# Performance work log

Measured on AMD Instinct MI355X. Metric: run time of the kernel, lower is better.

The kernel has to match this reference:

```python
import jax, jax.numpy as jnp
import numpy as np

THETA = 10000.0  # RoPE base


def _rope(x):
    # x: [B, T, H] with H even. Matches torch view_as_complex on (..., H//2, 2)
    # pairing of adjacent elements, rotated by m * theta_i.
    B, T, H = x.shape
    inv_freq = 1.0 / (THETA ** (jnp.arange(0, H, 2, dtype=jnp.float32) / H))  # [H/2]
    ang = jnp.arange(T, dtype=jnp.float32)[:, None] * inv_freq[None, :]       # [T, H/2]
    cos, sin = jnp.cos(ang), jnp.sin(ang)
    xr = x.astype(jnp.float32).reshape(B, T, H // 2, 2)
    a, b = xr[..., 0], xr[..., 1]
    out = jnp.stack([a * cos - b * sin, a * sin + b * cos], axis=-1)          # complex mult
    return out.reshape(B, T, H).astype(x.dtype)


def setup_inputs() -> dict:
    key = jax.random.key(0)
    k1, k2, k3, k4 = jax.random.split(key, 4)
    B, T, C, H = 4, 4096, 1024, 64
    return {
        "x": jax.random.normal(k1, (B, T, C), dtype=jnp.float32),
        "wq": jax.random.normal(k2, (C, H), dtype=jnp.float32) * 0.02,
        "wk": jax.random.normal(k3, (C, H), dtype=jnp.float32) * 0.02,
        "wv": jax.random.normal(k4, (C, H), dtype=jnp.float32) * 0.02,
    }


def reference(x, wq, wk, wv):
    # Head.forward, training branch; dropout is identity (eval determinism).
    B, T, C = x.shape
    H = wq.shape[1]
    q = _rope(x @ wq)   # [B, T, H]
    k = _rope(x @ wk)   # [B, T, H]
    v = x @ wv          # [B, T, H]
    wei = jnp.einsum('bqh,bkh->bqk', q, k) * (H ** -0.5)   # [B, T, T]
    causal = jnp.tril(jnp.ones((T, T), dtype=bool))
    wei = jnp.where(causal, wei, -jnp.inf)
    wei = jax.nn.softmax(wei, axis=-1)
    out = jnp.einsum('bqk,bkh->bqh', wei, v)               # [B, T, H]
    return out
```

## Files before the change

kernel.cpp:

```cpp
#include <hip/hip_runtime.h>
#include <hip/hip_bf16.h>
#include <math.h>

#define B_ 4
#define T_ 4096
#define C_ 1024
#define H_ 64
#define ROWS_ (B_*T_)

typedef __attribute__((ext_vector_type(8))) short bf16x8;
typedef __attribute__((ext_vector_type(4))) float f32x4;

__device__ __forceinline__ unsigned short f2bf(float f) {
    union { float f; unsigned u; } x; x.f = f;
    unsigned r = x.u + 0x7fffu + ((x.u >> 16) & 1u);
    return (unsigned short)(r >> 16);
}
__device__ __forceinline__ float bf2f(unsigned short s) {
    union { unsigned u; float f; } x; x.u = ((unsigned)s) << 16;
    return x.f;
}
__device__ __forceinline__ unsigned pk2bf(float a, float b) {
    __hip_bfloat162 h = __float22bfloat162_rn(float2{a, b});
    return *reinterpret_cast<unsigned*>(&h);
}
__device__ __forceinline__ void gld16(const void* g, void* l) {
    __builtin_amdgcn_global_load_lds(
        (const __attribute__((address_space(1))) unsigned*)g,
        (__attribute__((address_space(3))) unsigned*)l, 16, 0, 0);
}

__global__ __launch_bounds__(256) void prep_weights(
    const float* __restrict__ wq, const float* __restrict__ wk,
    const float* __restrict__ wv, unsigned short* __restrict__ wt)
{
    __shared__ float ts[64][68];
    const int m  = blockIdx.x >> 4;
    const int k0 = (blockIdx.x & 15) * 64;
    const float* w = (m == 0) ? wq : (m == 1) ? wk : wv;
    const int tid = threadIdx.x;
    {
        const int r = tid >> 2;
        const int c = (tid & 3) * 16;
        #pragma unroll
        for (int i = 0; i < 4; ++i)
            *reinterpret_cast<float4*>(&ts[r][c + 4*i]) =
                *reinterpret_cast<const float4*>(&w[(size_t)(k0 + r)*H_ + c + 4*i]);
    }
    __syncthreads();
    {
        const int n  = tid >> 2;
        const int kc = (tid & 3) * 16;
        unsigned short outp[16];
        #pragma unroll
        for (int j = 0; j < 16; ++j) outp[j] = f2bf(ts[kc + j][n]);
        unsigned short* dst = &wt[((size_t)m*64 + n)*C_ + k0 + kc];
        *reinterpret_cast<uint4*>(dst)     = *reinterpret_cast<uint4*>(&outp[0]);
        *reinterpret_cast<uint4*>(dst + 8) = *reinterpret_cast<uint4*>(&outp[8]);
    }
}

__global__ __launch_bounds__(256) void rope_table_kernel(float* __restrict__ tab)
{
    const int idx = blockIdx.x*256 + threadIdx.x;
    const int t   = idx >> 5;
    const int hp  = idx & 31;
    const float inv = __builtin_exp2f(-(float)hp * (13.287712379549449f / 32.f));
    float sn, cs;
    sincosf((float)t * inv, &sn, &cs);
    *reinterpret_cast<float2*>(&tab[2*idx]) = float2{cs, sn};
}

__global__ __launch_bounds__(512, 2) void qkv_mfma_kernel(
    const float* __restrict__ x, const unsigned short* __restrict__ wt,
    const float* __restrict__ tab,
    unsigned short* __restrict__ qb, unsigned short* __restrict__ kb,
    unsigned short* __restrict__ vtb)
{
    __shared__ unsigned short SM[32768];

    const int tid  = threadIdx.x;
    const int w    = tid >> 6;
    const int lane = tid & 63;
    const int rt   = w >> 1;
    const int ch   = w & 1;
    const int lr   = lane & 15;
    const int lg   = lane >> 4;
    const int rb   = blockIdx.x * 64;

    const int ar = tid >> 3;
    const int ac = (tid & 7) * 8;

    float4 axr[2];

    auto load_A = [&](int t) {
        const float* p = &x[(size_t)(rb + ar)*C_ + t*64 + ac];
        axr[0] = *reinterpret_cast<const float4*>(p);
        axr[1] = *reinterpret_cast<const float4*>(p + 4);
    };
    auto write_A = [&](int buf) {
        unsigned tmp[4];
        tmp[0] = pk2bf(axr[0].x, axr[0].y);
        tmp[1] = pk2bf(axr[0].z, axr[0].w);
        tmp[2] = pk2bf(axr[1].x, axr[1].y);
        tmp[3] = pk2bf(axr[1].z, axr[1].w);
        const int off = buf*8192 + ar*128 + ((ac*2) ^ ((ar & 7) << 4));
        *reinterpret_cast<uint4*>((char*)SM + off) = *reinterpret_cast<uint4*>(tmp);
    };
    auto stage_W = [&](int t, int buf) {
        #pragma unroll
        for (int s = 0; s < 3; ++s) {
            const int slot = s*512 + tid;
            const int r    = slot >> 3;
            const int c8   = (slot & 7) * 8;
            const int c8s  = c8 ^ ((r & 7) << 3);
            gld16(&wt[(size_t)r*C_ + t*64 + c8s],
                  (char*)SM + 16384 + buf*24576 + slot*16);
        }
    };

    f32x4 acc[6];
    #pragma unroll
    for (int j = 0; j < 6; ++j) acc[j] = f32x4{0.f, 0.f, 0.f, 0.f};

    load_A(0);
    stage_W(0, 0);
    write_A(0);
    load_A(1);

    for (int t = 0; t < 16; ++t) {
        const int cur = t & 1, nxt = cur ^ 1;
        __syncthreads();
        if (t < 15) { stage_W(t + 1, nxt); write_A(nxt); }
        if (t < 14) load_A(t + 2);
        char* Acur = (char*)SM + cur*8192;
        char* Wcur = (char*)SM + 16384 + cur*24576;
        #pragma unroll
        for (int kh = 0; kh < 2; ++kh) {
            const int arow = rt*16 + lr;
            bf16x8 af = *reinterpret_cast<const bf16x8*>(
                Acur + arow*128 + ((kh*64 + lg*16) ^ ((arow & 7) << 4)));
            #pragma unroll
            for (int j = 0; j < 6; ++j) {
                const int n = ch*96 + j*16 + lr;
                bf16x8 bf = *reinterpret_cast<const bf16x8*>(
                    Wcur + n*128 + ((kh*64 + lg*16) ^ ((n & 7) << 4)));
                acc[j] = __builtin_amdgcn_mfma_f32_16x16x32_bf16(af, bf, acc[j], 0, 0, 0);
            }
        }
    }

    __syncthreads();
    const int rl0  = rt*16 + lg*4;
    const int row0 = rb + rl0;
    #pragma unroll
    for (int j = 0; j < 6; ++j) {
        const int c = ch*96 + j*16 + lr;
        const int m = c >> 6;
        const int h = c & 63;
        if (m < 2) {
            const int base_ls = (m == 0) ? 0 : 4096;
            const float qs = (m == 0) ? 0.125f : 1.0f;
            const int hp = h >> 1;
            #pragma unroll
            for (int i = 0; i < 4; ++i) {
                const float v  = acc[j][i];
                const float pr = __shfl_xor(v, 1);
                if (!(h & 1)) {
                    const int tp = (row0 + i) & (T_ - 1);
                    const float2 cssn = *reinterpret_cast<const float2*>(
                        &tab[((size_t)tp*32 + hp)*2]);
                    const float oe = (v*cssn.x - pr*cssn.y) * qs;
                    const float oo = (v*cssn.y + pr*cssn.x) * qs;
                    *reinterpret_cast<unsigned*>(&SM[base_ls + (rl0 + i)*64 + h]) =
                        pk2bf(oe, oo);
                }
            }
        } else {
            unsigned short pk[4];
            #pragma unroll
            for (int i = 0; i < 4; ++i) pk[i] = f2bf(acc[j][i]);
            char* vbase = (char*)SM + 16384 + h*128;
            *reinterpret_cast<uint2*>(vbase + ((rl0*2) ^ ((h & 7) << 3))) =
                *reinterpret_cast<uint2*>(pk);
        }
    }
    __syncthreads();
    {
        const int row = tid >> 3;
        const int h0  = (tid & 7) * 8;
        *reinterpret_cast<uint4*>(&qb[(size_t)(rb + row)*H_ + h0]) =
            *reinterpret_cast<const uint4*>(&SM[row*64 + h0]);
        *reinterpret_cast<uint4*>(&kb[(size_t)(rb + row)*H_ + h0]) =
            *reinterpret_cast<const uint4*>(&SM[4096 + row*64 + h0]);
        const int h  = tid >> 3;
        const int t0 = (tid & 7) * 8;
        char* vbase = (char*)SM + 16384 + h*128;
        uint2 a  = *reinterpret_cast<uint2*>(vbase + (((t0*2)    ) ^ ((h & 7) << 3)));
        uint2 b2 = *reinterpret_cast<uint2*>(vbase + (((t0*2) + 8) ^ ((h & 7) << 3)));
        const int bh  = (rb >> 12)*64 + h;
        const int tp0 = rb & (T_ - 1);
        uint4 o; o.x = a.x; o.y = a.y; o.z = b2.x; o.w = b2.y;
        *reinterpret_cast<uint4*>(&vtb[(size_t)bh*T_ + tp0 + t0]) = o;
    }
}

__global__ __launch_bounds__(256, 4) void attn_chunk_kernel(
    const unsigned short* __restrict__ qb, const unsigned short* __restrict__ kb,
    const unsigned short* __restrict__ vtb,
    unsigned short* __restrict__ partO, float* __restrict__ partML,
    int CH, int per_batch)
{
    __shared__ unsigned short Kls[2][4096];
    __shared__ unsigned short Vls[2][4096];
    __shared__ unsigned short Pls[4][1024];

    const int tid  = threadIdx.x;
    const int w    = tid >> 6;
    const int lane = tid & 63;
    const int lr   = lane & 15;
    const int lg   = lane >> 4;

    const int cid = blockIdx.x;
    const int b   = cid / per_batch;
    int r0 = cid - b*per_batch;
    int g = 0, off = 0;
    while (r0 >= off + CH*(g + 1)) { off += CH*(g + 1); ++g; }
    const int idx = r0 - off;
    const int qt  = g*CH + idx/(g + 1);
    const int c   = idx % (g + 1);

    const int q0  = qt * 64;
    const int kt0 = c * CH;
    const int ns  = min(kt0 + CH, qt + 1) - kt0;
    const size_t rbase = (size_t)b * T_;

    char* Pw = (char*)&Pls[w][0];

    bf16x8 qf[2];
    {
        const unsigned short* qp = qb + (rbase + q0 + w*16 + lr)*H_ + lg*8;
        qf[0] = *reinterpret_cast<const bf16x8*>(qp);
        qf[1] = *reinterpret_cast<const bf16x8*>(qp + 32);
    }

    float mrow = -1e30f, lrow = 0.f;
    f32x4 acc[4];
    #pragma unroll
    for (int hs = 0; hs < 4; ++hs) acc[hs] = f32x4{0.f, 0.f, 0.f, 0.f};

    const int srow = tid >> 3;
    const int scol = (tid & 7) * 8;
    auto stage_dma = [&](int kt, int buf) {
        #pragma unroll
        for (int s = 0; s < 2; ++s) {
            const int r    = s*32 + srow;
            const int c8s  = scol ^ ((r & 7) << 3);
            const int slot = s*256 + tid;
            gld16(&kb[(rbase + (size_t)kt*64 + r)*H_ + c8s],
                  (char*)&Kls[buf][0] + slot*16);
            gld16(&vtb[((size_t)(b*64 + r))*T_ + (size_t)kt*64 + c8s],
                  (char*)&Vls[buf][0] + slot*16);
        }
    };

    stage_dma(kt0, 0);

    for (int s = 0; s < ns; ++s) {
        __syncthreads();
        if (s + 1 < ns) stage_dma(kt0 + s + 1, (s + 1) & 1);
        const int kt = kt0 + s;
        char* Kb = (char*)&Kls[s & 1][0];
        char* Vb = (char*)&Vls[s & 1][0];

        f32x4 st[4];
        __builtin_amdgcn_s_setprio(1);
        #pragma unroll
        for (int ks = 0; ks < 4; ++ks) {
            const int rr2 = ks*16 + lr;
            const int sw  = (rr2 & 7) << 4;
            bf16x8 kf0 = *reinterpret_cast<const bf16x8*>(Kb + rr2*128 + ((lg*16     ) ^ sw));
            bf16x8 kf1 = *reinterpret_cast<const bf16x8*>(Kb + rr2*128 + ((lg*16 + 64) ^ sw));
            f32x4 t = {0.f, 0.f, 0.f, 0.f};
            t = __builtin_amdgcn_mfma_f32_16x16x32_bf16(kf0, qf[0], t, 0, 0, 0);
            t = __builtin_amdgcn_mfma_f32_16x16x32_bf16(kf1, qf[1], t, 0, 0, 0);
            st[ks] = t;
        }
        __builtin_amdgcn_s_setprio(0);

        const int qg = q0 + w*16 + lr;
        float mx = -1e30f;
        if (kt == qt) {
            #pragma unroll
            for (int ks = 0; ks < 4; ++ks)
                #pragma unroll
                for (int i = 0; i < 4; ++i) {
                    const int kg = kt*64 + ks*16 + lg*4 + i;
                    const float v = (kg <= qg) ? st[ks][i] : -1e30f;
                    st[ks][i] = v;
                    mx = fmaxf(mx, v);
                }
        } else {
            #pragma unroll
            for (int ks = 0; ks < 4; ++ks)
                #pragma unroll
                for (int i = 0; i < 4; ++i) mx = fmaxf(mx, st[ks][i]);
        }
        mx = fmaxf(mx, __shfl_xor(mx, 16));
        mx = fmaxf(mx, __shfl_xor(mx, 32));
        const float mn  = fmaxf(mrow, mx);
        const float scl = __expf(mrow - mn);
        float ls = 0.f;
        #pragma unroll
        for (int ks = 0; ks < 4; ++ks)
            #pragma unroll
            for (int i = 0; i < 4; ++i) {
                const float p = __expf(st[ks][i] - mn);
                st[ks][i] = p;
                ls += p;
            }
        ls += __shfl_xor(ls, 16);
        ls += __shfl_xor(ls, 32);
        lrow = lrow*scl + ls;
        mrow = mn;

        const int swp = (lr & 7) << 4;
        #pragma unroll
        for (int ks = 0; ks < 4; ++ks) {
            const unsigned u0 = pk2bf(st[ks][0], st[ks][1]);
            const unsigned u1 = pk2bf(st[ks][2], st[ks][3]);
            *reinterpret_cast<uint2*>(Pw + lr*128 + ((ks*32 + lg*8) ^ swp)) =
                make_uint2(u0, u1);
        }

        float sclr[4];
        #pragma unroll
        for (int i = 0; i < 4; ++i) sclr[i] = __shfl(scl, lg*4 + i);
        #pragma unroll
        for (int hs = 0; hs < 4; ++hs)
            #pragma unroll
            for (int i = 0; i < 4; ++i) acc[hs][i] *= sclr[i];

        bf16x8 pf0 = *reinterpret_cast<const bf16x8*>(Pw + lr*128 + ((lg*16     ) ^ swp));
        bf16x8 pf1 = *reinterpret_cast<const bf16x8*>(Pw + lr*128 + ((lg*16 + 64) ^ swp));
        __builtin_amdgcn_s_setprio(1);
        #pragma unroll
        for (int hs = 0; hs < 4; ++hs) {
            const int rv  = hs*16 + lr;
            const int swv = (rv & 7) << 4;
            bf16x8 vf0 = *reinterpret_cast<const bf16x8*>(Vb + rv*128 + ((lg*16     ) ^ swv));
            bf16x8 vf1 = *reinterpret_cast<const bf16x8*>(Vb + rv*128 + ((lg*16 + 64) ^ swv));
            acc[hs] = __builtin_amdgcn_mfma_f32_16x16x32_bf16(pf0, vf0, acc[hs], 0, 0, 0);
            acc[hs] = __builtin_amdgcn_mfma_f32_16x16x32_bf16(pf1, vf1, acc[hs], 0, 0, 0);
        }
        __builtin_amdgcn_s_setprio(0);
    }

    const int myrow = w*16 + lr;
    if (lg == 0) {
        partML[(size_t)cid*128 + myrow]      = mrow;
        partML[(size_t)cid*128 + 64 + myrow] = lrow;
    }
    __syncthreads();
    unsigned short* Ols = &Kls[0][0];
    #pragma unroll
    for (int hs = 0; hs < 4; ++hs)
        #pragma unroll
        for (int i = 0; i < 4; ++i)
            Ols[(w*16 + lg*4 + i)*64 + hs*16 + lr] = f2bf(acc[hs][i]);
    __syncthreads();
    {
        const int e0 = tid * 16;
        *reinterpret_cast<uint4*>(&partO[(size_t)cid*4096 + e0]) =
            *reinterpret_cast<const uint4*>(&Ols[e0]);
        *reinterpret_cast<uint4*>(&partO[(size_t)cid*4096 + e0 + 8]) =
            *reinterpret_cast<const uint4*>(&Ols[e0 + 8]);
    }
}

__global__ __launch_bounds__(256) void combine_kernel(
    const unsigned short* __restrict__ partO, const float* __restrict__ partML,
    float* __restrict__ out, int CH, int per_batch)
{
    const int bq = blockIdx.x;
    const int b  = bq >> 6;
    const int qt = bq & 63;
    const int g  = qt / CH;
    const int nc = g + 1;
    const int cb = b*per_batch + (CH/2)*g*(g + 1) + (qt - g*CH)*(g + 1);

    const int tid = threadIdx.x;
    const int row = tid >> 2;
    const int h0  = (tid & 3) * 16;

    float mi[8], wi[8];
    float M = -1e30f;
    #pragma unroll
    for (int i = 0; i < 8; ++i) if (i < nc) {
        mi[i] = partML[(size_t)(cb + i)*128 + row];
        M = fmaxf(M, mi[i]);
    }
    float L = 0.f;
    #pragma unroll
    for (int i = 0; i < 8; ++i) if (i < nc) {
        wi[i] = __expf(mi[i] - M);
        L += partML[(size_t)(cb + i)*128 + 64 + row] * wi[i];
    }
    const float inv = 1.f / L;

    float o[16];
    #pragma unroll
    for (int j = 0; j < 16; ++j) o[j] = 0.f;
    #pragma unroll
    for (int i = 0; i < 8; ++i) if (i < nc) {
        const unsigned short* p = &partO[(size_t)(cb + i)*4096 + (size_t)row*64 + h0];
        uint4 u0 = *reinterpret_cast<const uint4*>(p);
        uint4 u1 = *reinterpret_cast<const uint4*>(p + 8);
        const unsigned* uu = (const unsigned*)&u0;
        #pragma unroll
        for (int j = 0; j < 4; ++j) {
            o[2*j]   += bf2f((unsigned short)(uu[j] & 0xffffu)) * wi[i];
            o[2*j+1] += bf2f((unsigned short)(uu[j] >> 16))     * wi[i];
        }
        const unsigned* uv = (const unsigned*)&u1;
        #pragma unroll
        for (int j = 0; j < 4; ++j) {
            o[8+2*j]   += bf2f((unsigned short)(uv[j] & 0xffffu)) * wi[i];
            o[8+2*j+1] += bf2f((unsigned short)(uv[j] >> 16))     * wi[i];
        }
    }
    float* op = &out[((size_t)b*T_ + (size_t)qt*64 + row)*H_ + h0];
    #pragma unroll
    for (int j = 0; j < 4; ++j) {
        float4 v = make_float4(o[4*j]*inv, o[4*j+1]*inv, o[4*j+2]*inv, o[4*j+3]*inv);
        *reinterpret_cast<float4*>(op + 4*j) = v;
    }
}

extern "C" void kernel_launch(void* const* d_in, const int* in_sizes, int n_in,
                              void* d_out, int out_size, void* d_ws, size_t ws_size,
                              hipStream_t stream) {
    const float* x  = (const float*)d_in[0];
    const float* wq = (const float*)d_in[1];
    const float* wk = (const float*)d_in[2];
    const float* wv = (const float*)d_in[3];
    float* out = (float*)d_out;

    unsigned short* qb  = (unsigned short*)d_ws;
    unsigned short* kb  = qb  + (size_t)ROWS_ * H_;
    unsigned short* vtb = kb  + (size_t)ROWS_ * H_;
    unsigned short* wt  = vtb + (size_t)ROWS_ * H_;

    const size_t fixed = (size_t)3*ROWS_*H_*2 + (size_t)3*64*C_*2;
    const size_t need8 = fixed + (size_t)1152*4096*2 + (size_t)1152*128*4;
    int CH, per_batch;
    if (ws_size >= need8) { CH = 8;  per_batch = 288; }
    else                  { CH = 16; per_batch = 160; }
    const int nblk = 4 * per_batch;

    unsigned short* partO  = wt + (size_t)3*64*C_;
    float*          partML = (float*)(partO + (size_t)nblk*4096);

    float* rope_tab = (float*)partO;

    prep_weights<<<48, 256, 0, stream>>>(wq, wk, wv, wt);
    rope_table_kernel<<<512, 256, 0, stream>>>(rope_tab);
    qkv_mfma_kernel<<<ROWS_/64, 512, 0, stream>>>(x, wt, rope_tab, qb, kb, vtb);
    attn_chunk_kernel<<<nblk, 256, 0, stream>>>(qb, kb, vtb, partO, partML,
                                                CH, per_batch);
    combine_kernel<<<256, 256, 0, stream>>>(partO, partML, out, CH, per_batch);
}
```

Before: 74.67 us.

## Double query tile per attention block and merge weight prep with RoPE table kernel

```diff
diff --git a/kernel.cpp b/kernel.cpp
--- a/kernel.cpp
+++ b/kernel.cpp
@@ -30,45 +30,45 @@
         (__attribute__((address_space(3))) unsigned*)l, 16, 0, 0);
 }
 
-__global__ __launch_bounds__(256) void prep_weights(
+__global__ __launch_bounds__(256) void prep_kernel(
     const float* __restrict__ wq, const float* __restrict__ wk,
-    const float* __restrict__ wv, unsigned short* __restrict__ wt)
+    const float* __restrict__ wv, unsigned short* __restrict__ wt,
+    float* __restrict__ tab)
 {
     __shared__ float ts[64][68];
-    const int m  = blockIdx.x >> 4;
-    const int k0 = (blockIdx.x & 15) * 64;
-    const float* w = (m == 0) ? wq : (m == 1) ? wk : wv;
     const int tid = threadIdx.x;
-    {
-        const int r = tid >> 2;
-        const int c = (tid & 3) * 16;
-        #pragma unroll
-        for (int i = 0; i < 4; ++i)
-            *reinterpret_cast<float4*>(&ts[r][c + 4*i]) =
-                *reinterpret_cast<const float4*>(&w[(size_t)(k0 + r)*H_ + c + 4*i]);
-    }
-    __syncthreads();
-    {
-        const int n  = tid >> 2;
-        const int kc = (tid & 3) * 16;
-        unsigned short outp[16];
-        #pragma unroll
-        for (int j = 0; j < 16; ++j) outp[j] = f2bf(ts[kc + j][n]);
-        unsigned short* dst = &wt[((size_t)m*64 + n)*C_ + k0 + kc];
-        *reinterpret_cast<uint4*>(dst)     = *reinterpret_cast<uint4*>(&outp[0]);
-        *reinterpret_cast<uint4*>(dst + 8) = *reinterpret_cast<uint4*>(&outp[8]);
-    }
-}
-
-__global__ __launch_bounds__(256) void rope_table_kernel(float* __restrict__ tab)
-{
-    const int idx = blockIdx.x*256 + threadIdx.x;
-    const int t   = idx >> 5;
-    const int hp  = idx & 31;
-    const float inv = __builtin_exp2f(-(float)hp * (13.287712379549449f / 32.f));
-    float sn, cs;
-    sincosf((float)t * inv, &sn, &cs);
-    *reinterpret_cast<float2*>(&tab[2*idx]) = float2{cs, sn};
+    if (blockIdx.x < 48) {
+        const int m  = blockIdx.x >> 4;
+        const int k0 = (blockIdx.x & 15) * 64;
+        const float* w = (m == 0) ? wq : (m == 1) ? wk : wv;
+        {
+            const int r = tid >> 2;
+            const int c = (tid & 3) * 16;
+            #pragma unroll
+            for (int i = 0; i < 4; ++i)
+                *reinterpret_cast<float4*>(&ts[r][c + 4*i]) =
+                    *reinterpret_cast<const float4*>(&w[(size_t)(k0 + r)*H_ + c + 4*i]);
+        }
+        __syncthreads();
+        {
+            const int n  = tid >> 2;
+            const int kc = (tid & 3) * 16;
+            unsigned short outp[16];
+            #pragma unroll
+            for (int j = 0; j < 16; ++j) outp[j] = f2bf(ts[kc + j][n]);
+            unsigned short* dst = &wt[((size_t)m*64 + n)*C_ + k0 + kc];
+            *reinterpret_cast<uint4*>(dst)     = *reinterpret_cast<uint4*>(&outp[0]);
+            *reinterpret_cast<uint4*>(dst + 8) = *reinterpret_cast<uint4*>(&outp[8]);
+        }
+    } else {
+        const int idx = (blockIdx.x - 48)*256 + tid;
+        const int t   = idx >> 5;
+        const int hp  = idx & 31;
+        const float inv = __builtin_exp2f(-(float)hp * (13.287712379549449f / 32.f));
+        float sn, cs;
+        sincosf((float)t * inv, &sn, &cs);
+        *reinterpret_cast<float2*>(&tab[2*idx]) = float2{cs, sn};
+    }
 }
 
 __global__ __launch_bounds__(512, 2) void qkv_mfma_kernel(
@@ -205,7 +205,7 @@
     }
 }
 
-__global__ __launch_bounds__(256, 4) void attn_chunk_kernel(
+__global__ __launch_bounds__(256, 3) void attn_chunk_kernel(
     const unsigned short* __restrict__ qb, const unsigned short* __restrict__ kb,
     const unsigned short* __restrict__ vtb,
     unsigned short* __restrict__ partO, float* __restrict__ partML,
@@ -213,7 +213,7 @@
 {
     __shared__ unsigned short Kls[2][4096];
     __shared__ unsigned short Vls[2][4096];
-    __shared__ unsigned short Pls[4][1024];
+    __shared__ unsigned short Pls[4][2048];
 
     const int tid  = threadIdx.x;
     const int w    = tid >> 6;
@@ -224,30 +224,37 @@
     const int cid = blockIdx.x;
     const int b   = cid / per_batch;
     int r0 = cid - b*per_batch;
-    int g = 0, off = 0;
-    while (r0 >= off + CH*(g + 1)) { off += CH*(g + 1); ++g; }
+    const int G = CH >> 1;
+    int a = 0, off = 0;
+    while (r0 >= off + G*(a + 1)) { off += G*(a + 1); ++a; }
     const int idx = r0 - off;
-    const int qt  = g*CH + idx/(g + 1);
-    const int c   = idx % (g + 1);
-
-    const int q0  = qt * 64;
+    const int qt  = G*a + idx/(a + 1);
+    const int c   = idx % (a + 1);
+
+    const int q0  = qt * 128;
     const int kt0 = c * CH;
-    const int ns  = min(kt0 + CH, qt + 1) - kt0;
+    const int ntk = 2*qt + 2;
+    const int ns  = min(kt0 + CH, ntk) - kt0;
     const size_t rbase = (size_t)b * T_;
+    const int dtile = 2*qt + (w >> 1);
 
     char* Pw = (char*)&Pls[w][0];
 
-    bf16x8 qf[2];
-    {
-        const unsigned short* qp = qb + (rbase + q0 + w*16 + lr)*H_ + lg*8;
-        qf[0] = *reinterpret_cast<const bf16x8*>(qp);
-        qf[1] = *reinterpret_cast<const bf16x8*>(qp + 32);
-    }
-
-    float mrow = -1e30f, lrow = 0.f;
-    f32x4 acc[4];
-    #pragma unroll
-    for (int hs = 0; hs < 4; ++hs) acc[hs] = f32x4{0.f, 0.f, 0.f, 0.f};
+    bf16x8 qf[2][2];
+    #pragma unroll
+    for (int s16 = 0; s16 < 2; ++s16) {
+        const unsigned short* qp = qb + (rbase + q0 + w*32 + s16*16 + lr)*H_ + lg*8;
+        qf[s16][0] = *reinterpret_cast<const bf16x8*>(qp);
+        qf[s16][1] = *reinterpret_cast<const bf16x8*>(qp + 32);
+    }
+
+    float mrow[2] = {-1e30f, -1e30f};
+    float lrow[2] = {0.f, 0.f};
+    f32x4 acc[2][4];
+    #pragma unroll
+    for (int s16 = 0; s16 < 2; ++s16)
+        #pragma unroll
+        for (int hs = 0; hs < 4; ++hs) acc[s16][hs] = f32x4{0.f, 0.f, 0.f, 0.f};
 
     const int srow = tid >> 3;
     const int scol = (tid & 7) * 8;
@@ -273,108 +280,135 @@
         char* Kb = (char*)&Kls[s & 1][0];
         char* Vb = (char*)&Vls[s & 1][0];
 
-        f32x4 st[4];
-        __builtin_amdgcn_s_setprio(1);
-        #pragma unroll
-        for (int ks = 0; ks < 4; ++ks) {
-            const int rr2 = ks*16 + lr;
-            const int sw  = (rr2 & 7) << 4;
-            bf16x8 kf0 = *reinterpret_cast<const bf16x8*>(Kb + rr2*128 + ((lg*16     ) ^ sw));
-            bf16x8 kf1 = *reinterpret_cast<const bf16x8*>(Kb + rr2*128 + ((lg*16 + 64) ^ sw));
-            f32x4 t = {0.f, 0.f, 0.f, 0.f};
-            t = __builtin_amdgcn_mfma_f32_16x16x32_bf16(kf0, qf[0], t, 0, 0, 0);
-            t = __builtin_amdgcn_mfma_f32_16x16x32_bf16(kf1, qf[1], t, 0, 0, 0);
-            st[ks] = t;
-        }
-        __builtin_amdgcn_s_setprio(0);
-
-        const int qg = q0 + w*16 + lr;
-        float mx = -1e30f;
-        if (kt == qt) {
-            #pragma unroll
-            for (int ks = 0; ks < 4; ++ks)
+        if (kt <= dtile) {
+            f32x4 st[2][4];
+            __builtin_amdgcn_s_setprio(1);
+            #pragma unroll
+            for (int ks = 0; ks < 4; ++ks) {
+                const int rr2 = ks*16 + lr;
+                const int sw  = (rr2 & 7) << 4;
+                bf16x8 kf0 = *reinterpret_cast<const bf16x8*>(Kb + rr2*128 + ((lg*16     ) ^ sw));
+                bf16x8 kf1 = *reinterpret_cast<const bf16x8*>(Kb + rr2*128 + ((lg*16 + 64) ^ sw));
                 #pragma unroll
-                for (int i = 0; i < 4; ++i) {
-                    const int kg = kt*64 + ks*16 + lg*4 + i;
-                    const float v = (kg <= qg) ? st[ks][i] : -1e30f;
-                    st[ks][i] = v;
-                    mx = fmaxf(mx, v);
+                for (int s16 = 0; s16 < 2; ++s16) {
+                    f32x4 t = {0.f, 0.f, 0.f, 0.f};
+                    t = __builtin_amdgcn_mfma_f32_16x16x32_bf16(kf0, qf[s16][0], t, 0, 0, 0);
+                    t = __builtin_amdgcn_mfma_f32_16x16x32_bf16(kf1, qf[s16][1], t, 0, 0, 0);
+                    st[s16][ks] = t;
                 }
-        } else {
-            #pragma unroll
-            for (int ks = 0; ks < 4; ++ks)
+            }
+            __builtin_amdgcn_s_setprio(0);
+
+            float scl[2];
+            const int swp = (lr & 7) << 4;
+            #pragma unroll
+            for (int s16 = 0; s16 < 2; ++s16) {
+                const int qg = q0 + w*32 + s16*16 + lr;
+                float mx = -1e30f;
+                if (kt == dtile) {
+                    #pragma unroll
+                    for (int ks = 0; ks < 4; ++ks)
+                        #pragma unroll
+                        for (int i = 0; i < 4; ++i) {
+                            const int kg = kt*64 + ks*16 + lg*4 + i;
+                            const float v = (kg <= qg) ? st[s16][ks][i] : -1e30f;
+                            st[s16][ks][i] = v;
+                            mx = fmaxf(mx, v);
+                        }
+                } else {
+                    #pragma unroll
+                    for (int ks = 0; ks < 4; ++ks)
+                        #pragma unroll
+                        for (int i = 0; i < 4; ++i) mx = fmaxf(mx, st[s16][ks][i]);
+                }
+                mx = fmaxf(mx, __shfl_xor(mx, 16));
+                mx = fmaxf(mx, __shfl_xor(mx, 32));
+                const float mn = fmaxf(mrow[s16], mx);
+                scl[s16] = __expf(mrow[s16] - mn);
+                float ls = 0.f;
                 #pragma unroll
-                for (int i = 0; i < 4; ++i) mx = fmaxf(mx, st[ks][i]);
-        }
-        mx = fmaxf(mx, __shfl_xor(mx, 16));
-        mx = fmaxf(mx, __shfl_xor(mx, 32));
-        const float mn  = fmaxf(mrow, mx);
-        const float scl = __expf(mrow - mn);
-        float ls = 0.f;
-        #pragma unroll
-        for (int ks = 0; ks < 4; ++ks)
-            #pragma unroll
-            for (int i = 0; i < 4; ++i) {
-                const float p = __expf(st[ks][i] - mn);
-                st[ks][i] = p;
-                ls += p;
-            }
-        ls += __shfl_xor(ls, 16);
-        ls += __shfl_xor(ls, 32);
-        lrow = lrow*scl + ls;
-        mrow = mn;
-
-        const int swp = (lr & 7) << 4;
-        #pragma unroll
-        for (int ks = 0; ks < 4; ++ks) {
-            const unsigned u0 = pk2bf(st[ks][0], st[ks][1]);
-            const unsigned u1 = pk2bf(st[ks][2], st[ks][3]);
-            *reinterpret_cast<uint2*>(Pw + lr*128 + ((ks*32 + lg*8) ^ swp)) =
-                make_uint2(u0, u1);
-        }
-
-        float sclr[4];
-        #pragma unroll
-        for (int i = 0; i < 4; ++i) sclr[i] = __shfl(scl, lg*4 + i);
-        #pragma unroll
-        for (int hs = 0; hs < 4; ++hs)
-            #pragma unroll
-            for (int i = 0; i < 4; ++i) acc[hs][i] *= sclr[i];
-
-        bf16x8 pf0 = *reinterpret_cast<const bf16x8*>(Pw + lr*128 + ((lg*16     ) ^ swp));
-        bf16x8 pf1 = *reinterpret_cast<const bf16x8*>(Pw + lr*128 + ((lg*16 + 64) ^ swp));
-        __builtin_amdgcn_s_setprio(1);
-        #pragma unroll
-        for (int hs = 0; hs < 4; ++hs) {
-            const int rv  = hs*16 + lr;
-            const int swv = (rv & 7) << 4;
-            bf16x8 vf0 = *reinterpret_cast<const bf16x8*>(Vb + rv*128 + ((lg*16     ) ^ swv));
-            bf16x8 vf1 = *reinterpret_cast<const bf16x8*>(Vb + rv*128 + ((lg*16 + 64) ^ swv));
-            acc[hs] = __builtin_amdgcn_mfma_f32_16x16x32_bf16(pf0, vf0, acc[hs], 0, 0, 0);
-            acc[hs] = __builtin_amdgcn_mfma_f32_16x16x32_bf16(pf1, vf1, acc[hs], 0, 0, 0);
-        }
-        __builtin_amdgcn_s_setprio(0);
-    }
-
-    const int myrow = w*16 + lr;
-    if (lg == 0) {
-        partML[(size_t)cid*128 + myrow]      = mrow;
-        partML[(size_t)cid*128 + 64 + myrow] = lrow;
+                for (int ks = 0; ks < 4; ++ks)
+                    #pragma unroll
+                    for (int i = 0; i < 4; ++i) {
+                        const float p = __expf(st[s16][ks][i] - mn);
+                        st[s16][ks][i] = p;
+                        ls += p;
+                    }
+                ls += __shfl_xor(ls, 16);
+                ls += __shfl_xor(ls, 32);
+                lrow[s16] = lrow[s16]*scl[s16] + ls;
+                mrow[s16] = mn;
+
+                const int pr = s16*16 + lr;
+                #pragma unroll
+                for (int ks = 0; ks < 4; ++ks) {
+                    const unsigned u0 = pk2bf(st[s16][ks][0], st[s16][ks][1]);
+                    const unsigned u1 = pk2bf(st[s16][ks][2], st[s16][ks][3]);
+                    *reinterpret_cast<uint2*>(Pw + pr*128 + ((ks*32 + lg*8) ^ swp)) =
+                        make_uint2(u0, u1);
+                }
+            }
+
+            #pragma unroll
+            for (int s16 = 0; s16 < 2; ++s16) {
+                float sclr[4];
+                #pragma unroll
+                for (int i = 0; i < 4; ++i) sclr[i] = __shfl(scl[s16], lg*4 + i);
+                #pragma unroll
+                for (int hs = 0; hs < 4; ++hs)
+                    #pragma unroll
+                    for (int i = 0; i < 4; ++i) acc[s16][hs][i] *= sclr[i];
+            }
+
+            bf16x8 pf[2][2];
+            #pragma unroll
+            for (int s16 = 0; s16 < 2; ++s16) {
+                const int pr = s16*16 + lr;
+                pf[s16][0] = *reinterpret_cast<const bf16x8*>(Pw + pr*128 + ((lg*16     ) ^ swp));
+                pf[s16][1] = *reinterpret_cast<const bf16x8*>(Pw + pr*128 + ((lg*16 + 64) ^ swp));
+            }
+            __builtin_amdgcn_s_setprio(1);
+            #pragma unroll
+            for (int hs = 0; hs < 4; ++hs) {
+                const int rv  = hs*16 + lr;
+                const int swv = (rv & 7) << 4;
+                bf16x8 vf0 = *reinterpret_cast<const bf16x8*>(Vb + rv*128 + ((lg*16     ) ^ swv));
+                bf16x8 vf1 = *reinterpret_cast<const bf16x8*>(Vb + rv*128 + ((lg*16 + 64) ^ swv));
+                #pragma unroll
+                for (int s16 = 0; s16 < 2; ++s16) {
+                    acc[s16][hs] = __builtin_amdgcn_mfma_f32_16x16x32_bf16(pf[s16][0], vf0, acc[s16][hs], 0, 0, 0);
+                    acc[s16][hs] = __builtin_amdgcn_mfma_f32_16x16x32_bf16(pf[s16][1], vf1, acc[s16][hs], 0, 0, 0);
+                }
+            }
+            __builtin_amdgcn_s_setprio(0);
+        }
+    }
+
+    #pragma unroll
+    for (int s16 = 0; s16 < 2; ++s16) {
+        const int myrow = w*32 + s16*16 + lr;
+        if (lg == 0) {
+            partML[(size_t)cid*256 + myrow]       = mrow[s16];
+            partML[(size_t)cid*256 + 128 + myrow] = lrow[s16];
+        }
     }
     __syncthreads();
     unsigned short* Ols = &Kls[0][0];
     #pragma unroll
-    for (int hs = 0; hs < 4; ++hs)
-        #pragma unroll
-        for (int i = 0; i < 4; ++i)
-            Ols[(w*16 + lg*4 + i)*64 + hs*16 + lr] = f2bf(acc[hs][i]);
+    for (int s16 = 0; s16 < 2; ++s16)
+        #pragma unroll
+        for (int hs = 0; hs < 4; ++hs)
+            #pragma unroll
+            for (int i = 0; i < 4; ++i)
+                Ols[(w*32 + s16*16 + lg*4 + i)*64 + hs*16 + lr] =
+                    f2bf(acc[s16][hs][i]);
     __syncthreads();
     {
-        const int e0 = tid * 16;
-        *reinterpret_cast<uint4*>(&partO[(size_t)cid*4096 + e0]) =
-            *reinterpret_cast<const uint4*>(&Ols[e0]);
-        *reinterpret_cast<uint4*>(&partO[(size_t)cid*4096 + e0 + 8]) =
-            *reinterpret_cast<const uint4*>(&Ols[e0 + 8]);
+        const int e0 = tid * 32;
+        #pragma unroll
+        for (int j = 0; j < 4; ++j)
+            *reinterpret_cast<uint4*>(&partO[(size_t)cid*8192 + e0 + 8*j]) =
+                *reinterpret_cast<const uint4*>(&Ols[e0 + 8*j]);
     }
 }
 
@@ -382,29 +416,31 @@
     const unsigned short* __restrict__ partO, const float* __restrict__ partML,
     float* __restrict__ out, int CH, int per_batch)
 {
-    const int bq = blockIdx.x;
-    const int b  = bq >> 6;
-    const int qt = bq & 63;
-    const int g  = qt / CH;
-    const int nc = g + 1;
-    const int cb = b*per_batch + (CH/2)*g*(g + 1) + (qt - g*CH)*(g + 1);
+    const int bq   = blockIdx.x;
+    const int b    = bq >> 6;
+    const int qt   = (bq >> 1) & 31;
+    const int half = bq & 1;
+    const int G  = CH >> 1;
+    const int a  = qt / G;
+    const int nc = a + 1;
+    const int cb = b*per_batch + (G*a*(a + 1))/2 + (qt - G*a)*(a + 1);
 
     const int tid = threadIdx.x;
-    const int row = tid >> 2;
+    const int row = half*64 + (tid >> 2);
     const int h0  = (tid & 3) * 16;
 
     float mi[8], wi[8];
     float M = -1e30f;
     #pragma unroll
     for (int i = 0; i < 8; ++i) if (i < nc) {
-        mi[i] = partML[(size_t)(cb + i)*128 + row];
+        mi[i] = partML[(size_t)(cb + i)*256 + row];
         M = fmaxf(M, mi[i]);
     }
     float L = 0.f;
     #pragma unroll
     for (int i = 0; i < 8; ++i) if (i < nc) {
         wi[i] = __expf(mi[i] - M);
-        L += partML[(size_t)(cb + i)*128 + 64 + row] * wi[i];
+        L += partML[(size_t)(cb + i)*256 + 128 + row] * wi[i];
     }
     const float inv = 1.f / L;
 
@@ -413,7 +449,7 @@
     for (int j = 0; j < 16; ++j) o[j] = 0.f;
     #pragma unroll
     for (int i = 0; i < 8; ++i) if (i < nc) {
-        const unsigned short* p = &partO[(size_t)(cb + i)*4096 + (size_t)row*64 + h0];
+        const unsigned short* p = &partO[(size_t)(cb + i)*8192 + (size_t)row*64 + h0];
         uint4 u0 = *reinterpret_cast<const uint4*>(p);
         uint4 u1 = *reinterpret_cast<const uint4*>(p + 8);
         const unsigned* uu = (const unsigned*)&u0;
@@ -429,7 +465,7 @@
             o[8+2*j+1] += bf2f((unsigned short)(uv[j] >> 16))     * wi[i];
         }
     }
-    float* op = &out[((size_t)b*T_ + (size_t)qt*64 + row)*H_ + h0];
+    float* op = &out[((size_t)b*T_ + (size_t)qt*128 + row)*H_ + h0];
     #pragma unroll
     for (int j = 0; j < 4; ++j) {
         float4 v = make_float4(o[4*j]*inv, o[4*j+1]*inv, o[4*j+2]*inv, o[4*j+3]*inv);
@@ -452,19 +488,18 @@
     unsigned short* wt  = vtb + (size_t)ROWS_ * H_;
 
     const size_t fixed = (size_t)3*ROWS_*H_*2 + (size_t)3*64*C_*2;
-    const size_t need8 = fixed + (size_t)1152*4096*2 + (size_t)1152*128*4;
+    const size_t need8 = fixed + (size_t)576*8192*2 + (size_t)576*256*4;
     int CH, per_batch;
-    if (ws_size >= need8) { CH = 8;  per_batch = 288; }
-    else                  { CH = 16; per_batch = 160; }
+    if (ws_size >= need8) { CH = 8;  per_batch = 144; }
+    else                  { CH = 16; per_batch = 80; }
     const int nblk = 4 * per_batch;
 
     unsigned short* partO  = wt + (size_t)3*64*C_;
-    float*          partML = (float*)(partO + (size_t)nblk*4096);
+    float*          partML = (float*)(partO + (size_t)nblk*8192);
 
     float* rope_tab = (float*)partO;
 
-    prep_weights<<<48, 256, 0, stream>>>(wq, wk, wv, wt);
-    rope_table_kernel<<<512, 256, 0, stream>>>(rope_tab);
+    prep_kernel<<<560, 256, 0, stream>>>(wq, wk, wv, wt, rope_tab);
     qkv_mfma_kernel<<<ROWS_/64, 512, 0, stream>>>(x, wt, rope_tab, qb, kb, vtb);
     attn_chunk_kernel<<<nblk, 256, 0, stream>>>(qb, kb, vtb, partO, partML,
                                                 CH, per_batch);
```

After: 74.08 us. About the same (-0.8%).
